# Kernel optimization log

Hardware: AMD Instinct MI355X
Metric: run time of the kernel (lower is better)

The kernel has to match this reference:

```python
import jax, jax.numpy as jnp
import numpy as np


def setup_inputs() -> dict:
    key = jax.random.key(0)
    k1, k2 = jax.random.split(key)
    C, H, W = 64, 1024, 1024
    NUM_SP = 2048
    x = jax.random.normal(k1, (C, H, W), dtype=jnp.float32)
    sp = jax.random.randint(k2, (H, W), 0, NUM_SP, dtype=jnp.int32)
    return {"x": x, "sp": sp, "num_segments": NUM_SP}


def reference(x, sp, num_segments):
    # x: [C, H, W], sp: [H, W] superpixel labels in [0, num_segments)
    C, H, W = x.shape
    N = H * W
    sp_flat = sp.reshape(N)                      # [N]
    x_flat = x.reshape(C, N).T                   # [N, C]
    # Per-superpixel, per-channel sums and pixel counts (single-pass segment reduce)
    sums = jax.ops.segment_sum(x_flat, sp_flat, num_segments=num_segments)   # [S, C]
    counts = jax.ops.segment_sum(jnp.ones((N,), dtype=x.dtype), sp_flat,
                                 num_segments=num_segments)                  # [S]
    means = sums / jnp.maximum(counts, 1.0)[:, None]                         # [S, C]
    # Broadcast each superpixel's mean back to its pixels
    out = means[sp_flat].T.reshape(C, H, W)
    return out
```

## Files before the change

### kernel.cpp

```cpp
#include <hip/hip_runtime.h>

#define NUM_SP 2048
#define NG_SUM 11
#define SUM_THREADS 1024
#define SUM_CHUNKS 46
#define BCAST_THREADS 512
#define BCAST_CHUNKS 64
#define NGB 8
#define FBITS 21
#define FMASK ((1ULL << FBITS) - 1ULL)
#define CNT_SHIFT 42


__global__ __launch_bounds__(256) void zero_kernel(float* ws, int n) {
    int i = blockIdx.x * 256 + threadIdx.x;
    int stride = gridDim.x * 256;
    for (; i < n; i += stride) ws[i] = 0.0f;
}

template <int CHN, bool WCNT>
__device__ __forceinline__ void sum_body(const float* __restrict__ xg,
                                         const int* __restrict__ sp,
                                         unsigned long long* __restrict__ acc,
                                         int base, int end, int N,
                                         float scale, float bsr) {
    for (int p = base + (int)threadIdx.x; p < end; p += SUM_THREADS) {
        int s = sp[p];
        float v[CHN];
#pragma unroll
        for (int c = 0; c < CHN; ++c) v[c] = xg[c * N + p];
        unsigned long long q0 = 0, q1 = 0;
#pragma unroll
        for (int c = 0; c < CHN; ++c) {
            unsigned long long u = (unsigned int)fmaf(v[c], scale, bsr);
            if (c < 3) q0 |= u << (c * FBITS);
            else       q1 |= u << ((c - 3) * FBITS);
        }
        if (WCNT) q1 |= (1ULL << CNT_SHIFT);
        atomicAdd(&acc[(s << 1) + 0], q0);
        atomicAdd(&acc[(s << 1) + 1], q1);
    }
}

__global__ __launch_bounds__(SUM_THREADS, 8) void sum_kernel(
        const float* __restrict__ x, const int* __restrict__ sp,
        unsigned long long* __restrict__ outq,
        int N, int chunks, int use_partials, float scale, float bsr) {
    __shared__ unsigned long long acc[NUM_SP * 2];
    for (int i = threadIdx.x; i < NUM_SP * 2; i += SUM_THREADS) acc[i] = 0ULL;
    __syncthreads();

    const int gs = blockIdx.y;
    const int chunk = blockIdx.x;
    const int per = (N + chunks - 1) / chunks;
    const int base = chunk * per;
    int end = base + per; if (end > N) end = N;
    const float* xg = x + (size_t)gs * 6 * N;

    if (gs == NG_SUM - 1) sum_body<4, true >(xg, sp, acc, base, end, N, scale, bsr);
    else                  sum_body<6, false>(xg, sp, acc, base, end, N, scale, bsr);
    __syncthreads();

    unsigned long long* dst = outq + (size_t)(use_partials ? (chunk * NG_SUM + gs) : gs)
                                     * (NUM_SP * 2);
    for (int i = threadIdx.x; i < NUM_SP * 2; i += SUM_THREADS) {
        unsigned long long v = acc[i];
        if (use_partials) dst[i] = v;
        else if (v) atomicAdd(&dst[i], v);
    }
}

__global__ __launch_bounds__(256) void cnt_kernel(const unsigned long long* __restrict__ partq,
                                                  float* __restrict__ counts, int chunks) {
    int s = blockIdx.x * 256 + threadIdx.x;
    if (s >= NUM_SP) return;
    unsigned long long c = 0;
    for (int k = 0; k < chunks; ++k)
        c += partq[(size_t)(k * NG_SUM + (NG_SUM - 1)) * (NUM_SP * 2) + (s << 1) + 1]
             >> CNT_SHIFT;
    counts[s] = (float)c;
}

__global__ __launch_bounds__(256) void mean_kernel(const unsigned long long* __restrict__ partq,
                                                   const float* __restrict__ counts,
                                                   float* __restrict__ means,
                                                   int SC, int chunks, float scale) {
    int i = blockIdx.x * 256 + threadIdx.x;
    if (i >= SC) return;
    int s = i & (NUM_SP - 1);
    int c = i >> 11;
    int gs = c / 6;
    int f = c - gs * 6;
    int j = f / 3, sub = f - j * 3;
    unsigned long long fs = 0;
    for (int k = 0; k < chunks; ++k) {
        unsigned long long q = partq[(size_t)(k * NG_SUM + gs) * (NUM_SP * 2) + (s << 1) + j];
        fs += (q >> (sub * FBITS)) & FMASK;
    }
    float cnt = counts[s];
    double sv = ((double)fs - (double)cnt * (double)(6.0f * scale)) / (double)scale;
    means[((size_t)(c >> 3) * NUM_SP + s) * 8 + (c & 7)] = (float)(sv / fmax((double)cnt, 1.0));
}

__global__ __launch_bounds__(BCAST_THREADS, 4) void bcast_kernel(
        const int* __restrict__ sp, const float4* __restrict__ means4,
        float* __restrict__ out, int N) {
    __shared__ float4 tbl[NUM_SP * 2];
    const int g = blockIdx.y;
    for (int e = threadIdx.x; e < NUM_SP * 2; e += BCAST_THREADS)
        tbl[e] = means4[(size_t)g * (NUM_SP * 2) + e];
    __syncthreads();

    int per = (N + gridDim.x - 1) / gridDim.x;
    per = (per + 3) & ~3;
    const int base = blockIdx.x * per;
    int end = base + per; if (end > N) end = N;
    if (end <= base) return;
    const int end4 = base + ((end - base) & ~3);

    const int4* sp4 = (const int4*)sp;
    float4* o0 = (float4*)(out + (size_t)(g * NGB + 0) * N);
    float4* o1 = (float4*)(out + (size_t)(g * NGB + 1) * N);
    float4* o2 = (float4*)(out + (size_t)(g * NGB + 2) * N);
    float4* o3 = (float4*)(out + (size_t)(g * NGB + 3) * N);
    float4* o4 = (float4*)(out + (size_t)(g * NGB + 4) * N);
    float4* o5 = (float4*)(out + (size_t)(g * NGB + 5) * N);
    float4* o6 = (float4*)(out + (size_t)(g * NGB + 6) * N);
    float4* o7 = (float4*)(out + (size_t)(g * NGB + 7) * N);

    for (int q = (base >> 2) + (int)threadIdx.x; q < (end4 >> 2); q += BCAST_THREADS) {
        int4 s4 = sp4[q];
        float4 ax = tbl[(s4.x << 1)], ay = tbl[(s4.x << 1) + 1];
        float4 bx = tbl[(s4.y << 1)], by = tbl[(s4.y << 1) + 1];
        float4 cx = tbl[(s4.z << 1)], cy = tbl[(s4.z << 1) + 1];
        float4 dx = tbl[(s4.w << 1)], dy = tbl[(s4.w << 1) + 1];
        o0[q] = make_float4(ax.x, bx.x, cx.x, dx.x);
        o1[q] = make_float4(ax.y, bx.y, cx.y, dx.y);
        o2[q] = make_float4(ax.z, bx.z, cx.z, dx.z);
        o3[q] = make_float4(ax.w, bx.w, cx.w, dx.w);
        o4[q] = make_float4(ay.x, by.x, cy.x, dy.x);
        o5[q] = make_float4(ay.y, by.y, cy.y, dy.y);
        o6[q] = make_float4(ay.z, by.z, cy.z, dy.z);
        o7[q] = make_float4(ay.w, by.w, cy.w, dy.w);
    }
    for (int p = end4 + (int)threadIdx.x; p < end; p += BCAST_THREADS) {
        int s = sp[p];
        float4 t0 = tbl[(s << 1)], t1 = tbl[(s << 1) + 1];
        out[(size_t)(g * NGB + 0) * N + p] = t0.x;
        out[(size_t)(g * NGB + 1) * N + p] = t0.y;
        out[(size_t)(g * NGB + 2) * N + p] = t0.z;
        out[(size_t)(g * NGB + 3) * N + p] = t0.w;
        out[(size_t)(g * NGB + 4) * N + p] = t1.x;
        out[(size_t)(g * NGB + 5) * N + p] = t1.y;
        out[(size_t)(g * NGB + 6) * N + p] = t1.z;
        out[(size_t)(g * NGB + 7) * N + p] = t1.w;
    }
}

extern "C" void kernel_launch(void* const* d_in, const int* in_sizes, int n_in,
                              void* d_out, int out_size, void* d_ws, size_t ws_size,
                              hipStream_t stream) {
    const float* x = (const float*)d_in[0];
    const int* sp = (const int*)d_in[1];
    const int N = in_sizes[1];
    const int C = in_sizes[0] / N;
    float* out = (float*)d_out;
    float* ws = (float*)d_ws;

    const int S = NUM_SP;
    const int SC = S * C;

    float* counts = ws;
    float* means = ws + S;
    unsigned long long* partq = (unsigned long long*)(ws + S + SC);

    const size_t part_floats_per_chunk = (size_t)NG_SUM * NUM_SP * 2 * 2;
    size_t ws_floats = ws_size / sizeof(float);
    size_t avail = (ws_floats > (size_t)(S + SC)) ? ws_floats - (size_t)(S + SC) : 0;
    int chunks = (int)(avail / part_floats_per_chunk);
    if (chunks > SUM_CHUNKS) chunks = SUM_CHUNKS;
    int use_partials = (chunks >= 32) ? 1 : 0;
    int grid_chunks = use_partials ? chunks : SUM_CHUNKS;
    float scale = use_partials ? 2048.0f : 128.0f;
    float bsr = 6.0f * scale + 0.5f;

    if (!use_partials) {
        zero_kernel<<<64, 256, 0, stream>>>((float*)partq, (int)part_floats_per_chunk);
    }
    dim3 g2(grid_chunks, NG_SUM);
    sum_kernel<<<g2, SUM_THREADS, 0, stream>>>(x, sp, partq, N, grid_chunks,
                                               use_partials, scale, bsr);
    int rchunks = use_partials ? grid_chunks : 1;
    cnt_kernel<<<NUM_SP / 256, 256, 0, stream>>>(partq, counts, rchunks);
    mean_kernel<<<(SC + 255) / 256, 256, 0, stream>>>(partq, counts, means, SC,
                                                      rchunks, scale);
    dim3 gb(BCAST_CHUNKS, NGB);
    bcast_kernel<<<gb, BCAST_THREADS, 0, stream>>>(sp, (const float4*)means, out, N);
}
```

Baseline: 495.0 us.

## Fuse sum, mean, and broadcast stages into one cooperative kernel with grid syncs

Adds a cooperative persistent kernel that performs the per-chunk segment sums, the mean reduction, and the broadcast in three phases separated by grid-wide syncs, replacing four separate launches. Counts are accumulated with float atomics during the sum phase instead of a separate count kernel. This is meant to remove launch overhead and inter-kernel gaps, at the cost of halved threads per block in the sum phase, grid sync latency, and a fixed 512-block grid. The older multi-kernel path remains as a fallback if cooperative launch fails.

```diff
diff --git a/kernel.cpp b/kernel.cpp
--- a/kernel.cpp
+++ b/kernel.cpp
@@ -1,15 +1,23 @@
 #include <hip/hip_runtime.h>
+#include <hip/hip_cooperative_groups.h>
 
 #define NUM_SP 2048
 #define NG_SUM 11
+#define FBITS 21
+#define FMASK ((1ULL << FBITS) - 1ULL)
+#define CNT_SHIFT 42
+
+#define CBLK 512
+#define CTHR 512
+#define CCHUNK 46
+#define CSCALE 2048.0f
+#define BCH 64
+#define NGB 8
+
 #define SUM_THREADS 1024
 #define SUM_CHUNKS 46
 #define BCAST_THREADS 512
 #define BCAST_CHUNKS 64
-#define NGB 8
-#define FBITS 21
-#define FMASK ((1ULL << FBITS) - 1ULL)
-#define CNT_SHIFT 42
 
 
 __global__ __launch_bounds__(256) void zero_kernel(float* ws, int n) {
@@ -18,13 +26,13 @@
     for (; i < n; i += stride) ws[i] = 0.0f;
 }
 
-template <int CHN, bool WCNT>
+template <int CHN, bool WCNT, int THREADS>
 __device__ __forceinline__ void sum_body(const float* __restrict__ xg,
                                          const int* __restrict__ sp,
                                          unsigned long long* __restrict__ acc,
                                          int base, int end, int N,
                                          float scale, float bsr) {
-    for (int p = base + (int)threadIdx.x; p < end; p += SUM_THREADS) {
+    for (int p = base + (int)threadIdx.x; p < end; p += THREADS) {
         int s = sp[p];
         float v[CHN];
 #pragma unroll
@@ -42,6 +50,111 @@
     }
 }
 
+__global__ __launch_bounds__(CTHR, 4) void fused_kernel(
+        const float* __restrict__ x, const int* __restrict__ sp,
+        unsigned long long* __restrict__ partq, float* __restrict__ counts,
+        float* __restrict__ means, float* __restrict__ out, int N) {
+    __shared__ float4 tbl[NUM_SP * 2];
+    unsigned long long* acc = (unsigned long long*)tbl;
+    cooperative_groups::grid_group grid = cooperative_groups::this_grid();
+    const int bid = blockIdx.x;
+    const int tid = threadIdx.x;
+
+    if (bid < CCHUNK * NG_SUM) {
+        for (int i = tid; i < NUM_SP * 2; i += CTHR) acc[i] = 0ULL;
+        __syncthreads();
+        const int chunk = bid / NG_SUM;
+        const int gs = bid - chunk * NG_SUM;
+        const int per = (N + CCHUNK - 1) / CCHUNK;
+        const int base = chunk * per;
+        int end = base + per; if (end > N) end = N;
+        const float* xg = x + (size_t)gs * 6 * N;
+        const float bsr = 6.0f * CSCALE + 0.5f;
+        if (gs == NG_SUM - 1) sum_body<4, true,  CTHR>(xg, sp, acc, base, end, N, CSCALE, bsr);
+        else                  sum_body<6, false, CTHR>(xg, sp, acc, base, end, N, CSCALE, bsr);
+        __syncthreads();
+        unsigned long long* dst = partq + (size_t)(chunk * NG_SUM + gs) * (NUM_SP * 2);
+        for (int i = tid; i < NUM_SP * 2; i += CTHR) dst[i] = acc[i];
+        if (gs == NG_SUM - 1) {
+            for (int s = tid; s < NUM_SP; s += CTHR)
+                atomicAdd(&counts[s], (float)(acc[(s << 1) + 1] >> CNT_SHIFT));
+        }
+    }
+    grid.sync();
+
+    {
+        int i = bid * CTHR + tid;
+        if (i < NUM_SP * 64) {
+            int s = i & (NUM_SP - 1);
+            int c = i >> 11;
+            int gs2 = c / 6;
+            int f = c - gs2 * 6;
+            int j = f / 3, sub = f - j * 3;
+            unsigned long long fs = 0;
+            for (int k = 0; k < CCHUNK; ++k)
+                fs += (partq[(size_t)(k * NG_SUM + gs2) * (NUM_SP * 2) + (s << 1) + j]
+                       >> (sub * FBITS)) & FMASK;
+            float cnt = counts[s];
+            double sv = ((double)fs - (double)cnt * (double)(6.0f * CSCALE)) / (double)CSCALE;
+            means[((size_t)(c >> 3) * NUM_SP + s) * 8 + (c & 7)] =
+                (float)(sv / fmax((double)cnt, 1.0));
+        }
+    }
+    grid.sync();
+
+    {
+        const int g = bid >> 6;
+        const int k = bid & 63;
+        const float4* m4 = (const float4*)means + (size_t)g * (NUM_SP * 2);
+        for (int e = tid; e < NUM_SP * 2; e += CTHR) tbl[e] = m4[e];
+        __syncthreads();
+
+        int per = (N + BCH - 1) / BCH;
+        per = (per + 3) & ~3;
+        const int base = k * per;
+        int end = base + per; if (end > N) end = N;
+        if (end > base) {
+            const int end4 = base + ((end - base) & ~3);
+            const int4* sp4 = (const int4*)sp;
+            float4* o0 = (float4*)(out + (size_t)(g * NGB + 0) * N);
+            float4* o1 = (float4*)(out + (size_t)(g * NGB + 1) * N);
+            float4* o2 = (float4*)(out + (size_t)(g * NGB + 2) * N);
+            float4* o3 = (float4*)(out + (size_t)(g * NGB + 3) * N);
+            float4* o4 = (float4*)(out + (size_t)(g * NGB + 4) * N);
+            float4* o5 = (float4*)(out + (size_t)(g * NGB + 5) * N);
+            float4* o6 = (float4*)(out + (size_t)(g * NGB + 6) * N);
+            float4* o7 = (float4*)(out + (size_t)(g * NGB + 7) * N);
+            for (int q = (base >> 2) + tid; q < (end4 >> 2); q += CTHR) {
+                int4 s4 = sp4[q];
+                float4 ax = tbl[(s4.x << 1)], ay = tbl[(s4.x << 1) + 1];
+                float4 bx = tbl[(s4.y << 1)], by = tbl[(s4.y << 1) + 1];
+                float4 cx = tbl[(s4.z << 1)], cy = tbl[(s4.z << 1) + 1];
+                float4 dx = tbl[(s4.w << 1)], dy = tbl[(s4.w << 1) + 1];
+                o0[q] = make_float4(ax.x, bx.x, cx.x, dx.x);
+                o1[q] = make_float4(ax.y, bx.y, cx.y, dx.y);
+                o2[q] = make_float4(ax.z, bx.z, cx.z, dx.z);
+                o3[q] = make_float4(ax.w, bx.w, cx.w, dx.w);
+                o4[q] = make_float4(ay.x, by.x, cy.x, dy.x);
+                o5[q] = make_float4(ay.y, by.y, cy.y, dy.y);
+                o6[q] = make_float4(ay.z, by.z, cy.z, dy.z);
+                o7[q] = make_float4(ay.w, by.w, cy.w, dy.w);
+            }
+            for (int p = end4 + tid; p < end; p += CTHR) {
+                int s = sp[p];
+                float4 t0 = tbl[(s << 1)], t1 = tbl[(s << 1) + 1];
+                out[(size_t)(g * NGB + 0) * N + p] = t0.x;
+                out[(size_t)(g * NGB + 1) * N + p] = t0.y;
+                out[(size_t)(g * NGB + 2) * N + p] = t0.z;
+                out[(size_t)(g * NGB + 3) * N + p] = t0.w;
+                out[(size_t)(g * NGB + 4) * N + p] = t1.x;
+                out[(size_t)(g * NGB + 5) * N + p] = t1.y;
+                out[(size_t)(g * NGB + 6) * N + p] = t1.z;
+                out[(size_t)(g * NGB + 7) * N + p] = t1.w;
+            }
+        }
+    }
+}
+
 __global__ __launch_bounds__(SUM_THREADS, 8) void sum_kernel(
         const float* __restrict__ x, const int* __restrict__ sp,
         unsigned long long* __restrict__ outq,
@@ -49,18 +162,15 @@
     __shared__ unsigned long long acc[NUM_SP * 2];
     for (int i = threadIdx.x; i < NUM_SP * 2; i += SUM_THREADS) acc[i] = 0ULL;
     __syncthreads();
-
     const int gs = blockIdx.y;
     const int chunk = blockIdx.x;
     const int per = (N + chunks - 1) / chunks;
     const int base = chunk * per;
     int end = base + per; if (end > N) end = N;
     const float* xg = x + (size_t)gs * 6 * N;
-
-    if (gs == NG_SUM - 1) sum_body<4, true >(xg, sp, acc, base, end, N, scale, bsr);
-    else                  sum_body<6, false>(xg, sp, acc, base, end, N, scale, bsr);
+    if (gs == NG_SUM - 1) sum_body<4, true,  SUM_THREADS>(xg, sp, acc, base, end, N, scale, bsr);
+    else                  sum_body<6, false, SUM_THREADS>(xg, sp, acc, base, end, N, scale, bsr);
     __syncthreads();
-
     unsigned long long* dst = outq + (size_t)(use_partials ? (chunk * NG_SUM + gs) : gs)
                                      * (NUM_SP * 2);
     for (int i = threadIdx.x; i < NUM_SP * 2; i += SUM_THREADS) {
@@ -110,14 +220,12 @@
     for (int e = threadIdx.x; e < NUM_SP * 2; e += BCAST_THREADS)
         tbl[e] = means4[(size_t)g * (NUM_SP * 2) + e];
     __syncthreads();
-
     int per = (N + gridDim.x - 1) / gridDim.x;
     per = (per + 3) & ~3;
     const int base = blockIdx.x * per;
     int end = base + per; if (end > N) end = N;
     if (end <= base) return;
     const int end4 = base + ((end - base) & ~3);
-
     const int4* sp4 = (const int4*)sp;
     float4* o0 = (float4*)(out + (size_t)(g * NGB + 0) * N);
     float4* o1 = (float4*)(out + (size_t)(g * NGB + 1) * N);
@@ -127,7 +235,6 @@
     float4* o5 = (float4*)(out + (size_t)(g * NGB + 5) * N);
     float4* o6 = (float4*)(out + (size_t)(g * NGB + 6) * N);
     float4* o7 = (float4*)(out + (size_t)(g * NGB + 7) * N);
-
     for (int q = (base >> 2) + (int)threadIdx.x; q < (end4 >> 2); q += BCAST_THREADS) {
         int4 s4 = sp4[q];
         float4 ax = tbl[(s4.x << 1)], ay = tbl[(s4.x << 1) + 1];
@@ -178,12 +285,23 @@
     size_t ws_floats = ws_size / sizeof(float);
     size_t avail = (ws_floats > (size_t)(S + SC)) ? ws_floats - (size_t)(S + SC) : 0;
     int chunks = (int)(avail / part_floats_per_chunk);
+
+    if (chunks >= CCHUNK && C == 64 && (N & 3) == 0) {
+        zero_kernel<<<8, 256, 0, stream>>>(counts, S);
+        void* args[] = {(void*)&x, (void*)&sp, (void*)&partq, (void*)&counts,
+                        (void*)&means, (void*)&out, (void*)&N};
+        hipError_t e = hipLaunchCooperativeKernel((const void*)fused_kernel,
+                                                  dim3(CBLK), dim3(CTHR),
+                                                  args, 0, stream);
+        if (e == hipSuccess) return;
+        (void)hipGetLastError();
+    }
+
     if (chunks > SUM_CHUNKS) chunks = SUM_CHUNKS;
     int use_partials = (chunks >= 32) ? 1 : 0;
     int grid_chunks = use_partials ? chunks : SUM_CHUNKS;
     float scale = use_partials ? 2048.0f : 128.0f;
     float bsr = 6.0f * scale + 0.5f;
-
     if (!use_partials) {
         zero_kernel<<<64, 256, 0, stream>>>((float*)partq, (int)part_floats_per_chunk);
     }
```

After: 612.8 us. 1.24x slower.

## Vectorize sum loads to pairs and regroup broadcast into 4-channel groups

Applied to the files above, without the earlier changes.

The sum kernel now processes two pixels per thread using int2/float2 loads and issues four shared atomics per iteration, with a serial tail for odd counts. Chunk boundaries are rounded to even sizes. The broadcast kernel switches from 8-channel to 4-channel groups (16 blocks in y, 256 threads, 32 KB LDS table), and the means layout changes to match. The aim is wider global loads in the reduction and a smaller LDS footprint for higher occupancy in the broadcast. The cost is that the sp labels are re-read twice as often.

```diff
diff --git a/kernel.cpp b/kernel.cpp
--- a/kernel.cpp
+++ b/kernel.cpp
@@ -4,9 +4,9 @@
 #define NG_SUM 11
 #define SUM_THREADS 1024
 #define SUM_CHUNKS 46
-#define BCAST_THREADS 512
+#define BCAST_THREADS 256
 #define BCAST_CHUNKS 64
-#define NGB 8
+#define NGB 4
 #define FBITS 21
 #define FMASK ((1ULL << FBITS) - 1ULL)
 #define CNT_SHIFT 42
@@ -18,27 +18,50 @@
     for (; i < n; i += stride) ws[i] = 0.0f;
 }
 
-template <int CHN, bool WCNT>
-__device__ __forceinline__ void sum_body(const float* __restrict__ xg,
-                                         const int* __restrict__ sp,
-                                         unsigned long long* __restrict__ acc,
-                                         int base, int end, int N,
-                                         float scale, float bsr) {
-    for (int p = base + (int)threadIdx.x; p < end; p += SUM_THREADS) {
-        int s = sp[p];
-        float v[CHN];
+template <int CHN, bool WCNT, int THREADS>
+__device__ __forceinline__ void sum_body_pair(const float* __restrict__ xg,
+                                              const int* __restrict__ sp,
+                                              unsigned long long* __restrict__ acc,
+                                              int base, int end, int N,
+                                              float scale, float bsr) {
+    const int2* sp2 = (const int2*)sp;
+    const int i0 = base >> 1;
+    const int i1 = (end - base) >= 2 ? ((base + ((end - base) & ~1)) >> 1) : i0;
+    for (int i = i0 + (int)threadIdx.x; i < i1; i += THREADS) {
+        int2 ss = sp2[i];
+        float2 v[CHN];
 #pragma unroll
-        for (int c = 0; c < CHN; ++c) v[c] = xg[c * N + p];
-        unsigned long long q0 = 0, q1 = 0;
+        for (int c = 0; c < CHN; ++c)
+            v[c] = ((const float2*)(xg + (size_t)c * N))[i];
+        unsigned long long qa0 = 0, qa1 = 0, qb0 = 0, qb1 = 0;
 #pragma unroll
         for (int c = 0; c < CHN; ++c) {
-            unsigned long long u = (unsigned int)fmaf(v[c], scale, bsr);
-            if (c < 3) q0 |= u << (c * FBITS);
-            else       q1 |= u << ((c - 3) * FBITS);
+            unsigned long long ua = (unsigned int)fmaf(v[c].x, scale, bsr);
+            unsigned long long ub = (unsigned int)fmaf(v[c].y, scale, bsr);
+            if (c < 3) { qa0 |= ua << (c * FBITS); qb0 |= ub << (c * FBITS); }
+            else       { qa1 |= ua << ((c - 3) * FBITS); qb1 |= ub << ((c - 3) * FBITS); }
         }
-        if (WCNT) q1 |= (1ULL << CNT_SHIFT);
-        atomicAdd(&acc[(s << 1) + 0], q0);
-        atomicAdd(&acc[(s << 1) + 1], q1);
+        if (WCNT) { qa1 |= (1ULL << CNT_SHIFT); qb1 |= (1ULL << CNT_SHIFT); }
+        atomicAdd(&acc[(ss.x << 1) + 0], qa0);
+        atomicAdd(&acc[(ss.x << 1) + 1], qa1);
+        atomicAdd(&acc[(ss.y << 1) + 0], qb0);
+        atomicAdd(&acc[(ss.y << 1) + 1], qb1);
+    }
+    int tail = base + ((end - base) & ~1);
+    if (threadIdx.x == 0) {
+        for (int p = tail; p < end; ++p) {
+            int s = sp[p];
+            unsigned long long q0 = 0, q1 = 0;
+#pragma unroll
+            for (int c = 0; c < CHN; ++c) {
+                unsigned long long u = (unsigned int)fmaf(xg[(size_t)c * N + p], scale, bsr);
+                if (c < 3) q0 |= u << (c * FBITS);
+                else       q1 |= u << ((c - 3) * FBITS);
+            }
+            if (WCNT) q1 |= (1ULL << CNT_SHIFT);
+            atomicAdd(&acc[(s << 1) + 0], q0);
+            atomicAdd(&acc[(s << 1) + 1], q1);
+        }
     }
 }
 
@@ -49,18 +72,20 @@
     __shared__ unsigned long long acc[NUM_SP * 2];
     for (int i = threadIdx.x; i < NUM_SP * 2; i += SUM_THREADS) acc[i] = 0ULL;
     __syncthreads();
-
     const int gs = blockIdx.y;
     const int chunk = blockIdx.x;
-    const int per = (N + chunks - 1) / chunks;
+    int per = (N + chunks - 1) / chunks;
+    per = (per + 1) & ~1;
     const int base = chunk * per;
     int end = base + per; if (end > N) end = N;
-    const float* xg = x + (size_t)gs * 6 * N;
-
-    if (gs == NG_SUM - 1) sum_body<4, true >(xg, sp, acc, base, end, N, scale, bsr);
-    else                  sum_body<6, false>(xg, sp, acc, base, end, N, scale, bsr);
+    if (end > base) {
+        const float* xg = x + (size_t)gs * 6 * N;
+        if (gs == NG_SUM - 1)
+            sum_body_pair<4, true,  SUM_THREADS>(xg, sp, acc, base, end, N, scale, bsr);
+        else
+            sum_body_pair<6, false, SUM_THREADS>(xg, sp, acc, base, end, N, scale, bsr);
+    }
     __syncthreads();
-
     unsigned long long* dst = outq + (size_t)(use_partials ? (chunk * NG_SUM + gs) : gs)
                                      * (NUM_SP * 2);
     for (int i = threadIdx.x; i < NUM_SP * 2; i += SUM_THREADS) {
@@ -99,16 +124,16 @@
     }
     float cnt = counts[s];
     double sv = ((double)fs - (double)cnt * (double)(6.0f * scale)) / (double)scale;
-    means[((size_t)(c >> 3) * NUM_SP + s) * 8 + (c & 7)] = (float)(sv / fmax((double)cnt, 1.0));
-}
-
-__global__ __launch_bounds__(BCAST_THREADS, 4) void bcast_kernel(
+    means[((size_t)(c >> 2) * NUM_SP + s) * 4 + (c & 3)] = (float)(sv / fmax((double)cnt, 1.0));
+}
+
+__global__ __launch_bounds__(BCAST_THREADS, 5) void bcast_kernel(
         const int* __restrict__ sp, const float4* __restrict__ means4,
         float* __restrict__ out, int N) {
-    __shared__ float4 tbl[NUM_SP * 2];
+    __shared__ float4 tbl[NUM_SP];
     const int g = blockIdx.y;
-    for (int e = threadIdx.x; e < NUM_SP * 2; e += BCAST_THREADS)
-        tbl[e] = means4[(size_t)g * (NUM_SP * 2) + e];
+    for (int e = threadIdx.x; e < NUM_SP; e += BCAST_THREADS)
+        tbl[e] = means4[(size_t)g * NUM_SP + e];
     __syncthreads();
 
     int per = (N + gridDim.x - 1) / gridDim.x;
@@ -123,37 +148,24 @@
     float4* o1 = (float4*)(out + (size_t)(g * NGB + 1) * N);
     float4* o2 = (float4*)(out + (size_t)(g * NGB + 2) * N);
     float4* o3 = (float4*)(out + (size_t)(g * NGB + 3) * N);
-    float4* o4 = (float4*)(out + (size_t)(g * NGB + 4) * N);
-    float4* o5 = (float4*)(out + (size_t)(g * NGB + 5) * N);
-    float4* o6 = (float4*)(out + (size_t)(g * NGB + 6) * N);
-    float4* o7 = (float4*)(out + (size_t)(g * NGB + 7) * N);
 
     for (int q = (base >> 2) + (int)threadIdx.x; q < (end4 >> 2); q += BCAST_THREADS) {
         int4 s4 = sp4[q];
-        float4 ax = tbl[(s4.x << 1)], ay = tbl[(s4.x << 1) + 1];
-        float4 bx = tbl[(s4.y << 1)], by = tbl[(s4.y << 1) + 1];
-        float4 cx = tbl[(s4.z << 1)], cy = tbl[(s4.z << 1) + 1];
-        float4 dx = tbl[(s4.w << 1)], dy = tbl[(s4.w << 1) + 1];
-        o0[q] = make_float4(ax.x, bx.x, cx.x, dx.x);
-        o1[q] = make_float4(ax.y, bx.y, cx.y, dx.y);
-        o2[q] = make_float4(ax.z, bx.z, cx.z, dx.z);
-        o3[q] = make_float4(ax.w, bx.w, cx.w, dx.w);
-        o4[q] = make_float4(ay.x, by.x, cy.x, dy.x);
-        o5[q] = make_float4(ay.y, by.y, cy.y, dy.y);
-        o6[q] = make_float4(ay.z, by.z, cy.z, dy.z);
-        o7[q] = make_float4(ay.w, by.w, cy.w, dy.w);
+        float4 a = tbl[s4.x];
+        float4 b = tbl[s4.y];
+        float4 c = tbl[s4.z];
+        float4 d = tbl[s4.w];
+        o0[q] = make_float4(a.x, b.x, c.x, d.x);
+        o1[q] = make_float4(a.y, b.y, c.y, d.y);
+        o2[q] = make_float4(a.z, b.z, c.z, d.z);
+        o3[q] = make_float4(a.w, b.w, c.w, d.w);
     }
     for (int p = end4 + (int)threadIdx.x; p < end; p += BCAST_THREADS) {
-        int s = sp[p];
-        float4 t0 = tbl[(s << 1)], t1 = tbl[(s << 1) + 1];
-        out[(size_t)(g * NGB + 0) * N + p] = t0.x;
-        out[(size_t)(g * NGB + 1) * N + p] = t0.y;
-        out[(size_t)(g * NGB + 2) * N + p] = t0.z;
-        out[(size_t)(g * NGB + 3) * N + p] = t0.w;
-        out[(size_t)(g * NGB + 4) * N + p] = t1.x;
-        out[(size_t)(g * NGB + 5) * N + p] = t1.y;
-        out[(size_t)(g * NGB + 6) * N + p] = t1.z;
-        out[(size_t)(g * NGB + 7) * N + p] = t1.w;
+        float4 m = tbl[sp[p]];
+        out[(size_t)(g * NGB + 0) * N + p] = m.x;
+        out[(size_t)(g * NGB + 1) * N + p] = m.y;
+        out[(size_t)(g * NGB + 2) * N + p] = m.z;
+        out[(size_t)(g * NGB + 3) * N + p] = m.w;
     }
 }
 
@@ -194,6 +206,6 @@
     cnt_kernel<<<NUM_SP / 256, 256, 0, stream>>>(partq, counts, rchunks);
     mean_kernel<<<(SC + 255) / 256, 256, 0, stream>>>(partq, counts, means, SC,
                                                       rchunks, scale);
-    dim3 gb(BCAST_CHUNKS, NGB);
+    dim3 gb(BCAST_CHUNKS, C / NGB);
     bcast_kernel<<<gb, BCAST_THREADS, 0, stream>>>(sp, (const float4*)means, out, N);
 }
```

After: 493.8 us. Within noise of the previous version (-0.3%).
